# Kernel optimization log

Measured on AMD Instinct MI355X. Metric: run time of the kernel, lower is better.

## Reference

```python
import jax, jax.numpy as jnp
import numpy as np
from jax import lax

B, T, S_ENC = 64, 32, 64
E, H, V = 1024, 1024, 32000


def setup_inputs() -> dict:
    key = jax.random.key(0)
    ks = jax.random.split(key, 12)
    s = 0.02
    return {
        "inputs": jax.random.randint(ks[0], (B, T), 0, V),
        "encoder_outputs": jax.random.normal(ks[1], (B, S_ENC, 2 * H), jnp.float32),
        "h0": jax.random.normal(ks[2], (B, H), jnp.float32) * 0.1,
        "c0": jax.random.normal(ks[3], (B, H), jnp.float32) * 0.1,
        "emb": jax.random.normal(ks[4], (V, E), jnp.float32) * s,
        "W_ih": jax.random.normal(ks[5], (4 * H, E), jnp.float32) * s,
        "W_hh": jax.random.normal(ks[6], (4 * H, H), jnp.float32) * s,
        "b_ih": jnp.zeros((4 * H,), jnp.float32),
        "b_hh": jnp.zeros((4 * H,), jnp.float32),
        "attn_W": jax.random.normal(ks[7], (2 * H, H), jnp.float32) * s,  # Linear(H -> 2H, no bias)
        "comb_W": jax.random.normal(ks[8], (H, 3 * H), jnp.float32) * s,  # Linear(3H -> H)
        "comb_b": jnp.zeros((H,), jnp.float32),
        "out_W": jax.random.normal(ks[9], (V, H), jnp.float32) * s,       # Linear(H -> V)
        "out_b": jnp.zeros((V,), jnp.float32),
    }


def _decode(inputs, encoder_outputs, h0, c0, emb, W_ih, W_hh, b_ih, b_hh,
            attn_W, comb_W, comb_b, out_W, out_b):
    x = emb[inputs]                      # [B, T, E]
    bias = b_ih + b_hh

    def step(carry, x_t):
        h, c = carry                     # [B, H] each
        gates = x_t @ W_ih.T + h @ W_hh.T + bias    # [B, 4H]
        i, f, g, o = jnp.split(gates, 4, axis=-1)   # PyTorch LSTM gate order
        i, f, o = jax.nn.sigmoid(i), jax.nn.sigmoid(f), jax.nn.sigmoid(o)
        c = f * c + i * jnp.tanh(g)
        h = o * jnp.tanh(c)
        # Luong-style attention (faithful to source, incl. softmax over dim=1 of size 1)
        ah = h @ attn_W.T                                        # [B, 2H]
        scores = jnp.einsum('bd,bsd->bs', ah, encoder_outputs)[:, None, :]  # [B,1,S]
        w = jax.nn.softmax(scores, axis=1)                       # size-1 axis -> all ones
        ctx = jnp.einsum('bqs,bsd->bqd', w, encoder_outputs)[:, 0]          # [B, 2H]
        merged = jnp.concatenate([h, ctx], axis=-1)              # [B, 3H]
        out = jnp.tanh(merged @ comb_W.T + comb_b)               # [B, H]
        return (h, c), out

    (h, c), outs = lax.scan(step, (h0, c0), x.transpose(1, 0, 2))
    outputs = outs.transpose(1, 0, 2)                            # [B, T, H]
    logits = outputs @ out_W.T + out_b                           # [B, T, V]
    return logits, h, c


def reference(inputs, encoder_outputs, h0, c0, emb, W_ih, W_hh, b_ih, b_hh,
              attn_W, comb_W, comb_b, out_W, out_b):
    return _decode(inputs, encoder_outputs, h0, c0, emb, W_ih, W_hh, b_ih, b_hh,
                   attn_W, comb_W, comb_b, out_W, out_b)
```

## Files before the change

### kernel.cpp

```cpp
#include <hip/hip_runtime.h>
#include <hip/hip_bf16.h>


typedef unsigned short u16;
typedef unsigned int u32;
typedef short s8v __attribute__((ext_vector_type(8)));
typedef float f4v __attribute__((ext_vector_type(4)));

__device__ __forceinline__ u16 f2bf(float f) {
  unsigned x = __float_as_uint(f);
  return (u16)((x + 0x7fffu + ((x >> 16) & 1u)) >> 16);
}
__device__ __forceinline__ float bf2f(u16 u) {
  return __uint_as_float(((unsigned)u) << 16);
}

__device__ __forceinline__ void gl_lds16(const void* g, void* l) {
  __builtin_amdgcn_global_load_lds(
      (const __attribute__((address_space(1))) u32*)g,
      (__attribute__((address_space(3))) u32*)l, 16, 0, 0);
}

__device__ __forceinline__ int xcd_swz(int bid, int nb) {
  int q8 = nb >> 3, r8 = nb & 7;
  int xcd = bid & 7, idx = bid >> 3;
  return (xcd < r8 ? xcd * (q8 + 1) : r8 * (q8 + 1) + (xcd - r8) * q8) + idx;
}

template <int EPI>
__global__ __launch_bounds__(512, 1) void gemm_q(
    const u16* __restrict__ A, const u16* __restrict__ Bm,
    const float* __restrict__ bias, void* __restrict__ Cp,
    int K, int ldc, int gridM) {
  __shared__ __align__(16) u16 LDS[2 * 32768];

  int swz = xcd_swz((int)blockIdx.x, (int)gridDim.x);
  int mt = swz % gridM, nt = swz / gridM;
  long bm = (long)mt * 256, bn = (long)nt * 256;

  int tid = threadIdx.x;
  int w = tid >> 6, l = tid & 63;
  int wm = w & 1, wn = w >> 1;
  int lr = l & 15, lg = l >> 4;

  int nt_k = K >> 6;

  auto stage = [&](int s, int kt_idx) {
    int kt = kt_idx << 6;
    u16* sa = &LDS[s * 32768];
    u16* sb = &LDS[s * 32768 + 16384];
#pragma unroll
    for (int ch = 0; ch < 4; ++ch) {
      int cb = ch * 512 + w * 64;
      int c = cb + l;
      int row = c >> 3, sp = c & 7;
      int ko = kt + ((sp ^ (row & 7)) << 3);
      gl_lds16(A + (bm + row) * (long)K + ko, sa + cb * 8);
      gl_lds16(Bm + (bn + row) * (long)K + ko, sb + cb * 8);
    }
  };

  f4v acc[8][4];
#pragma unroll
  for (int i = 0; i < 8; ++i)
#pragma unroll
    for (int j = 0; j < 4; ++j) acc[i][j] = (f4v){0.f, 0.f, 0.f, 0.f};

  stage(0, 0);
  asm volatile("s_waitcnt vmcnt(0)" ::: "memory");
  __builtin_amdgcn_s_barrier();
  __builtin_amdgcn_sched_barrier(0);

  for (int t = 0; t < nt_k; ++t) {
    if (t + 1 < nt_k) stage((t + 1) & 1, t + 1);
    const u16* sa = &LDS[(t & 1) * 32768];
    const u16* sb = &LDS[(t & 1) * 32768 + 16384];
#pragma unroll
    for (int ks = 0; ks < 2; ++ks) {
      s8v av[8], bv[4];
#pragma unroll
      for (int i = 0; i < 8; ++i) {
        int ra = wm * 128 + i * 16 + lr;
        int pa = (ks * 4 + lg) ^ (ra & 7);
        av[i] = *(const s8v*)((const char*)sa + ra * 128 + pa * 16);
      }
#pragma unroll
      for (int i = 0; i < 4; ++i) {
        int rb = wn * 64 + i * 16 + lr;
        int pb = (ks * 4 + lg) ^ (rb & 7);
        bv[i] = *(const s8v*)((const char*)sb + rb * 128 + pb * 16);
      }
      __builtin_amdgcn_s_setprio(1);
#pragma unroll
      for (int mi = 0; mi < 8; ++mi)
#pragma unroll
        for (int ni = 0; ni < 4; ++ni)
          acc[mi][ni] = __builtin_amdgcn_mfma_f32_16x16x32_bf16(
              av[mi], bv[ni], acc[mi][ni], 0, 0, 0);
      __builtin_amdgcn_s_setprio(0);
    }
    if (t + 1 >= nt_k) break;
    asm volatile("s_waitcnt vmcnt(0)" ::: "memory");
    __builtin_amdgcn_s_barrier();
    __builtin_amdgcn_sched_barrier(0);
  }

#pragma unroll
  for (int mi = 0; mi < 8; ++mi) {
#pragma unroll
    for (int q = 0; q < 4; ++q) {
      long row = bm + wm * 128 + mi * 16 + lg * 4 + q;
#pragma unroll
      for (int ni = 0; ni < 4; ++ni) {
        long col = bn + wn * 64 + ni * 16 + lr;
        float v = acc[mi][ni][q] + bias[col];
        if (EPI == 3)
          ((float*)Cp)[row * (long)ldc + col] = v;
        else
          ((u16*)Cp)[row * (long)ldc + col] = f2bf(v);
      }
    }
  }
}

template <int EPI>
__global__ __launch_bounds__(512, 1) void gemm_p(
    const u16* __restrict__ A, const u16* __restrict__ Bm,
    const float* __restrict__ bias, void* __restrict__ Cp,
    int K, int ldc, int gridM) {
  __shared__ __align__(16) u16 LDS[3 * 24576];

  int swz = xcd_swz((int)blockIdx.x, (int)gridDim.x);
  int mt = swz % gridM, nt = swz / gridM;
  long bm = (long)mt * 128, bn = (long)nt * 256;

  int tid = threadIdx.x;
  int w = tid >> 6, l = tid & 63;
  int wm = w & 1, wn = w >> 1;
  int lr = l & 15, lg = l >> 4;

  int nt_k = K >> 6;

  auto stage = [&](int s, int kt_idx) {
    int kt = kt_idx << 6;
    u16* sa = &LDS[s * 24576];
    u16* sb = &LDS[s * 24576 + 8192];
#pragma unroll
    for (int ch = 0; ch < 2; ++ch) {
      int cb = ch * 512 + w * 64;
      int c = cb + l;
      int row = c >> 3, sp = c & 7;
      gl_lds16(A + (bm + row) * (long)K + kt + ((sp ^ (row & 7)) << 3),
               sa + cb * 8);
    }
#pragma unroll
    for (int ch = 0; ch < 4; ++ch) {
      int cb = ch * 512 + w * 64;
      int c = cb + l;
      int row = c >> 3, sp = c & 7;
      gl_lds16(Bm + (bn + row) * (long)K + kt + ((sp ^ (row & 7)) << 3),
               sb + cb * 8);
    }
  };

  f4v acc[4][4];
#pragma unroll
  for (int i = 0; i < 4; ++i)
#pragma unroll
    for (int j = 0; j < 4; ++j) acc[i][j] = (f4v){0.f, 0.f, 0.f, 0.f};

  stage(0, 0);
  stage(1, 1);
  asm volatile("s_waitcnt vmcnt(6)" ::: "memory");
  __builtin_amdgcn_s_barrier();
  __builtin_amdgcn_sched_barrier(0);

  for (int t = 0; t < nt_k; ++t) {
    if (t + 2 < nt_k) stage((t + 2) % 3, t + 2);
    const u16* sa = &LDS[(t % 3) * 24576];
    const u16* sb = &LDS[(t % 3) * 24576 + 8192];
#pragma unroll
    for (int ks = 0; ks < 2; ++ks) {
      s8v av[4], bv[4];
#pragma unroll
      for (int i = 0; i < 4; ++i) {
        int ra = wm * 64 + i * 16 + lr;
        int pa = (ks * 4 + lg) ^ (ra & 7);
        av[i] = *(const s8v*)((const char*)sa + ra * 128 + pa * 16);
        int rb = wn * 64 + i * 16 + lr;
        int pb = (ks * 4 + lg) ^ (rb & 7);
        bv[i] = *(const s8v*)((const char*)sb + rb * 128 + pb * 16);
      }
      __builtin_amdgcn_s_setprio(1);
#pragma unroll
      for (int mi = 0; mi < 4; ++mi)
#pragma unroll
        for (int ni = 0; ni < 4; ++ni)
          acc[mi][ni] = __builtin_amdgcn_mfma_f32_16x16x32_bf16(
              av[mi], bv[ni], acc[mi][ni], 0, 0, 0);
      __builtin_amdgcn_s_setprio(0);
    }
    if (t + 1 >= nt_k) break;
    if (t + 2 < nt_k) {
      asm volatile("s_waitcnt vmcnt(6)" ::: "memory");
    } else {
      asm volatile("s_waitcnt vmcnt(0)" ::: "memory");
    }
    __builtin_amdgcn_s_barrier();
    __builtin_amdgcn_sched_barrier(0);
  }

#pragma unroll
  for (int mi = 0; mi < 4; ++mi) {
#pragma unroll
    for (int q = 0; q < 4; ++q) {
      long row = bm + wm * 64 + mi * 16 + lg * 4 + q;
#pragma unroll
      for (int ni = 0; ni < 4; ++ni) {
        long col = bn + wn * 64 + ni * 16 + lr;
        float v = acc[mi][ni][q] + bias[col];
        if (EPI == 3)
          ((float*)Cp)[row * (long)ldc + col] = v;
        else
          ((u16*)Cp)[row * (long)ldc + col] = f2bf(v);
      }
    }
  }
}

template <int EPI>
__global__ __launch_bounds__(256, 2) void gemm_bt2(
    const u16* __restrict__ A, const u16* __restrict__ Bm,
    const float* __restrict__ bias, void* __restrict__ Cp,
    int K, int ldc, int gridM) {
  __shared__ __align__(16) u16 As[128 * 64];
  __shared__ __align__(16) u16 Bs[128 * 64];

  int swz = xcd_swz((int)blockIdx.x, (int)gridDim.x);
  int mt = swz % gridM, nt = swz / gridM;
  long bm = (long)mt * 128, bn = (long)nt * 128;

  int tid = threadIdx.x;
  int w = tid >> 6, l = tid & 63;
  int wm = (w & 1) * 64, wn = (w >> 1) * 64;
  int lr = l & 15, lg = l >> 4;

  f4v acc[4][4];
#pragma unroll
  for (int i = 0; i < 4; ++i)
#pragma unroll
    for (int j = 0; j < 4; ++j) acc[i][j] = (f4v){0.f, 0.f, 0.f, 0.f};

  for (int kt = 0; kt < K; kt += 64) {
#pragma unroll
    for (int p = 0; p < 4; ++p) {
      int cb = (p * 4 + w) * 64;
      int c = cb + l;
      int row = c >> 3, ce = (c & 7) * 8;
      gl_lds16(A + (bm + row) * (long)K + kt + ce, &As[cb * 8]);
      gl_lds16(Bm + (bn + row) * (long)K + kt + ce, &Bs[cb * 8]);
    }
    __syncthreads();
#pragma unroll
    for (int ks = 0; ks < 2; ++ks) {
      int kb = ks * 64 + lg * 16;
      s8v av[4], bv[4];
#pragma unroll
      for (int i = 0; i < 4; ++i) {
        av[i] = *(const s8v*)((const char*)&As[0] + (wm + i * 16 + lr) * 128 + kb);
        bv[i] = *(const s8v*)((const char*)&Bs[0] + (wn + i * 16 + lr) * 128 + kb);
      }
#pragma unroll
      for (int mi = 0; mi < 4; ++mi)
#pragma unroll
        for (int ni = 0; ni < 4; ++ni)
          acc[mi][ni] = __builtin_amdgcn_mfma_f32_16x16x32_bf16(
              av[mi], bv[ni], acc[mi][ni], 0, 0, 0);
    }
    __syncthreads();
  }
#pragma unroll
  for (int mi = 0; mi < 4; ++mi) {
#pragma unroll
    for (int q = 0; q < 4; ++q) {
      long row = bm + wm + mi * 16 + lg * 4 + q;
#pragma unroll
      for (int ni = 0; ni < 4; ++ni) {
        long col = bn + wn + ni * 16 + lr;
        float v = acc[mi][ni][q] + bias[col];
        if (EPI == 2) v = tanhf(v);
        if (EPI == 3)
          ((float*)Cp)[row * (long)ldc + col] = v;
        else
          ((u16*)Cp)[row * (long)ldc + col] = f2bf(v);
      }
    }
  }
}

template <int EPI>
__global__ __launch_bounds__(256, 2) void gemm_btf(
    const u16* __restrict__ A, const float* __restrict__ Bm,
    const float* __restrict__ bias, void* __restrict__ Cp,
    int K, int ldc, int gridM) {
  __shared__ __align__(16) u16 As[128][72];
  __shared__ __align__(16) u16 Bs[128][72];
  int swz = xcd_swz((int)blockIdx.x, (int)gridDim.x);
  int mt = swz % gridM, nt = swz / gridM;
  long bm = (long)mt * 128, bn = (long)nt * 128;
  int tid = threadIdx.x;
  int w = tid >> 6, l = tid & 63;
  int wm = (w & 1) * 64, wn = (w >> 1) * 64;
  int lr = l & 15, lg = l >> 4;
  f4v acc[4][4];
#pragma unroll
  for (int i = 0; i < 4; ++i)
#pragma unroll
    for (int j = 0; j < 4; ++j) acc[i][j] = (f4v){0.f, 0.f, 0.f, 0.f};
  for (int kt = 0; kt < K; kt += 64) {
#pragma unroll
    for (int p = 0; p < 4; ++p) {
      int ch = p * 256 + tid;
      int row = ch >> 3, cc = ch & 7;
      *(uint4*)((char*)(&As[0][0]) + row * 144 + cc * 16) =
          *(const uint4*)(A + (bm + row) * (long)K + kt + cc * 8);
      const float* bp = Bm + (bn + row) * (long)K + kt + cc * 8;
      float4 b0 = *(const float4*)bp;
      float4 b1 = *(const float4*)(bp + 4);
      union { u16 t8[8]; uint4 v; } cv;
      cv.t8[0] = f2bf(b0.x); cv.t8[1] = f2bf(b0.y);
      cv.t8[2] = f2bf(b0.z); cv.t8[3] = f2bf(b0.w);
      cv.t8[4] = f2bf(b1.x); cv.t8[5] = f2bf(b1.y);
      cv.t8[6] = f2bf(b1.z); cv.t8[7] = f2bf(b1.w);
      *(uint4*)((char*)(&Bs[0][0]) + row * 144 + cc * 16) = cv.v;
    }
    __syncthreads();
#pragma unroll
    for (int ks = 0; ks < 2; ++ks) {
      int kb = ks * 64 + lg * 16;
      s8v av[4], bv[4];
#pragma unroll
      for (int i = 0; i < 4; ++i) {
        av[i] = *(const s8v*)((const char*)(&As[0][0]) + (wm + i * 16 + lr) * 144 + kb);
        bv[i] = *(const s8v*)((const char*)(&Bs[0][0]) + (wn + i * 16 + lr) * 144 + kb);
      }
#pragma unroll
      for (int mi = 0; mi < 4; ++mi)
#pragma unroll
        for (int ni = 0; ni < 4; ++ni)
          acc[mi][ni] = __builtin_amdgcn_mfma_f32_16x16x32_bf16(
              av[mi], bv[ni], acc[mi][ni], 0, 0, 0);
    }
    __syncthreads();
  }
#pragma unroll
  for (int mi = 0; mi < 4; ++mi) {
#pragma unroll
    for (int q = 0; q < 4; ++q) {
      long row = bm + wm + mi * 16 + lg * 4 + q;
#pragma unroll
      for (int ni = 0; ni < 4; ++ni) {
        long col = bn + wn + ni * 16 + lr;
        float v = acc[mi][ni][q] + bias[col];
        if (EPI == 2) v = tanhf(v);
        if (EPI == 3)
          ((float*)Cp)[row * (long)ldc + col] = v;
        else
          ((u16*)Cp)[row * (long)ldc + col] = f2bf(v);
      }
    }
  }
}

__global__ __launch_bounds__(256, 1) void lstm_step3(
    const u16* __restrict__ Whh, const u16* __restrict__ xproj,
    const u16* __restrict__ h_in, u16* __restrict__ h_next,
    float* __restrict__ c_buf, u16* __restrict__ a2,
    float* __restrict__ hf, float* __restrict__ cf, int t) {
  __shared__ __align__(16) u16 Hs[32 * 1024];
  __shared__ __align__(16) u16 Ws[32 * 1024];
  __shared__ float Gs[32][33];

  int bid = blockIdx.x;
  int j = bid & 127, bh = bid >> 7;
  int colbase = j * 8;
  int tid = threadIdx.x, w = tid >> 6, l = tid & 63;
  int bq = w & 1, nh = w >> 1;
  int lr = l & 15, lg = l >> 4;

  int hi = tid >> 7;
  int ps = tid & 127;
#pragma unroll
  for (int p = 0; p < 16; ++p) {
    int r = 2 * p + hi;
    int sl = ps ^ (r & 7);
    gl_lds16(h_in + (bh * 32 + r) * 1024 + sl * 8, &Hs[(p * 4 + w) * 512]);
    int g = r >> 3, rr = r & 7;
    gl_lds16(Whh + (long)(g * 1024 + colbase + rr) * 1024 + sl * 8,
             &Ws[(p * 4 + w) * 512]);
  }
  __syncthreads();

  int ar = bq * 16 + lr;
  int br = nh * 16 + lr;
  int axor = (ar & 7), bxor = (br & 7);
  f4v acc0 = {0.f, 0.f, 0.f, 0.f}, acc1 = {0.f, 0.f, 0.f, 0.f};
#pragma unroll
  for (int kc = 0; kc < 32; kc += 2) {
    {
      int s = kc * 4 + lg;
      s8v av = *(const s8v*)((const char*)Hs + ar * 2048 + (s ^ axor) * 16);
      s8v bv = *(const s8v*)((const char*)Ws + br * 2048 + (s ^ bxor) * 16);
      acc0 = __builtin_amdgcn_mfma_f32_16x16x32_bf16(av, bv, acc0, 0, 0, 0);
    }
    {
      int s = (kc + 1) * 4 + lg;
      s8v av = *(const s8v*)((const char*)Hs + ar * 2048 + (s ^ axor) * 16);
      s8v bv = *(const s8v*)((const char*)Ws + br * 2048 + (s ^ bxor) * 16);
      acc1 = __builtin_amdgcn_mfma_f32_16x16x32_bf16(av, bv, acc1, 0, 0, 0);
    }
  }
#pragma unroll
  for (int q = 0; q < 4; ++q)
    Gs[bq * 16 + lg * 4 + q][nh * 16 + lr] = acc0[q] + acc1[q];
  __syncthreads();

  int b = tid >> 3, rr = tid & 7;
  int gb = bh * 32 + b;
  int col = colbase + rr;
  const u16* xp = xproj + (long)(gb * 32 + t) * 4096;
  float pi = Gs[b][rr]      + bf2f(xp[col]);
  float pf = Gs[b][8 + rr]  + bf2f(xp[1024 + col]);
  float pg = Gs[b][16 + rr] + bf2f(xp[2048 + col]);
  float po = Gs[b][24 + rr] + bf2f(xp[3072 + col]);
  float iv = 1.f / (1.f + expf(-pi));
  float fv = 1.f / (1.f + expf(-pf));
  float ov = 1.f / (1.f + expf(-po));
  float gv = tanhf(pg);
  float co = c_buf[gb * 1024 + col];
  float cn = fv * co + iv * gv;
  float hn = ov * tanhf(cn);
  c_buf[gb * 1024 + col] = cn;
  u16 hb = f2bf(hn);
  h_next[gb * 1024 + col] = hb;
  a2[(long)(gb * 32 + t) * 3072 + col] = hb;
  if (t == 31) {
    hf[gb * 1024 + col] = hn;
    cf[gb * 1024 + col] = cn;
  }
}

__global__ void k_misc(const float* __restrict__ bih, const float* __restrict__ bhh,
                       const float* __restrict__ h0, const float* __restrict__ c0,
                       float* __restrict__ bias, u16* __restrict__ hbuf0,
                       float* __restrict__ cbuf) {
  int i = blockIdx.x * 256 + threadIdx.x;
  if (i < 4096) bias[i] = bih[i] + bhh[i];
  if (i < 65536) {
    hbuf0[i] = f2bf(h0[i]);
    cbuf[i] = c0[i];
  }
}

__global__ void k_cvt8(const float* __restrict__ src, u16* __restrict__ dst, int n8) {
  int i = blockIdx.x * 256 + threadIdx.x;
  if (i >= n8) return;
  const float4* s = (const float4*)(src + (long)i * 8);
  float4 a = s[0], b = s[1];
  union { u16 t[8]; uint4 v; } cv;
  cv.t[0] = f2bf(a.x); cv.t[1] = f2bf(a.y); cv.t[2] = f2bf(a.z); cv.t[3] = f2bf(a.w);
  cv.t[4] = f2bf(b.x); cv.t[5] = f2bf(b.y); cv.t[6] = f2bf(b.z); cv.t[7] = f2bf(b.w);
  ((uint4*)dst)[i] = cv.v;
}

__global__ void k_emb8(const int* __restrict__ inp, const float* __restrict__ emb,
                       u16* __restrict__ dst) {
  int i = blockIdx.x * 256 + threadIdx.x;
  int r = i >> 7, k8 = (i & 127) * 8;
  const float* s = emb + (long)inp[r] * 1024 + k8;
  float4 a = *(const float4*)s, b = *(const float4*)(s + 4);
  union { u16 t[8]; uint4 v; } cv;
  cv.t[0] = f2bf(a.x); cv.t[1] = f2bf(a.y); cv.t[2] = f2bf(a.z); cv.t[3] = f2bf(a.w);
  cv.t[4] = f2bf(b.x); cv.t[5] = f2bf(b.y); cv.t[6] = f2bf(b.z); cv.t[7] = f2bf(b.w);
  ((uint4*)dst)[i] = cv.v;
}

__global__ void k_ctx2(const float* __restrict__ enc, u16* __restrict__ a2) {
  int b = blockIdx.x;
  int dg = threadIdx.x;
  float s[8] = {0.f, 0.f, 0.f, 0.f, 0.f, 0.f, 0.f, 0.f};
  for (int si = 0; si < 64; ++si) {
    const float* p = enc + ((long)(b * 64 + si)) * 2048 + dg * 8;
    float4 x = *(const float4*)p, y = *(const float4*)(p + 4);
    s[0] += x.x; s[1] += x.y; s[2] += x.z; s[3] += x.w;
    s[4] += y.x; s[5] += y.y; s[6] += y.z; s[7] += y.w;
  }
  union { u16 t[8]; uint4 v; } cv;
#pragma unroll
  for (int e = 0; e < 8; ++e) cv.t[e] = f2bf(s[e]);
  for (int t = 0; t < 32; ++t)
    *(uint4*)(a2 + (long)(b * 32 + t) * 3072 + 1024 + dg * 8) = cv.v;
}

extern "C" void kernel_launch(void* const* d_in, const int* in_sizes, int n_in,
                              void* d_out, int out_size, void* d_ws, size_t ws_size,
                              hipStream_t stream) {
  (void)in_sizes; (void)n_in; (void)out_size;
  const int*   inputs = (const int*)d_in[0];
  const float* enc    = (const float*)d_in[1];
  const float* h0     = (const float*)d_in[2];
  const float* c0     = (const float*)d_in[3];
  const float* emb    = (const float*)d_in[4];
  const float* Wih    = (const float*)d_in[5];
  const float* Whh    = (const float*)d_in[6];
  const float* bih    = (const float*)d_in[7];
  const float* bhh    = (const float*)d_in[8];
  const float* combW  = (const float*)d_in[10];
  const float* combb  = (const float*)d_in[11];
  const float* outW   = (const float*)d_in[12];
  const float* outb   = (const float*)d_in[13];
  float* out = (float*)d_out;

  char* ws = (char*)d_ws;
  size_t off = 0;
  auto alloc = [&](size_t bytes) {
    char* p = ws + off;
    off += (bytes + 255) & ~(size_t)255;
    return p;
  };
  u16*   WHH_BF = (u16*)  alloc(4096ull * 1024 * 2);
  u16*   XPROJ  = (u16*)  alloc(2048ull * 4096 * 2);
  u16*   EMBX   = (u16*)  alloc(2048ull * 1024 * 2);
  u16*   A2     = (u16*)  alloc(2048ull * 3072 * 2);
  u16*   OUTS   = (u16*)  alloc(2048ull * 1024 * 2);
  float* BIAS   = (float*)alloc(4096 * 4);
  u16*   HBUF   = (u16*)  alloc(2ull * 65536 * 2);
  float* CBUF   = (float*)alloc(65536 * 4);
  u16*   WIH_BF   = (u16*)alloc(4096ull * 1024 * 2);
  u16*   COMBW_BF = (u16*)alloc(1024ull * 3072 * 2);
  size_t off_w1 = off;
  u16*   OUTW_BF  = (u16*)alloc(32000ull * 1024 * 2);
  size_t off_w2 = off;
  bool haveW1 = ws_size >= off_w1;
  bool haveW2 = ws_size >= off_w2;

  k_misc<<<dim3(256), dim3(256), 0, stream>>>(bih, bhh, h0, c0, BIAS, HBUF, CBUF);
  k_cvt8<<<dim3(2048), dim3(256), 0, stream>>>(Whh, WHH_BF, 524288);
  k_emb8<<<dim3(1024), dim3(256), 0, stream>>>(inputs, emb, EMBX);
  k_ctx2<<<dim3(64), dim3(256), 0, stream>>>(enc, A2);
  if (haveW1) {
    k_cvt8<<<dim3(2048), dim3(256), 0, stream>>>(Wih, WIH_BF, 524288);
    k_cvt8<<<dim3(1536), dim3(256), 0, stream>>>(combW, COMBW_BF, 393216);
  }
  if (haveW2)
    k_cvt8<<<dim3(16000), dim3(256), 0, stream>>>(outW, OUTW_BF, 4096000);

  if (haveW1)
    gemm_p<1><<<dim3(256), dim3(512), 0, stream>>>(EMBX, WIH_BF, BIAS, XPROJ,
                                                   1024, 4096, 16);
  else
    gemm_btf<1><<<dim3(512), dim3(256), 0, stream>>>(EMBX, Wih, BIAS, XPROJ,
                                                     1024, 4096, 16);

  for (int t = 0; t < 32; ++t) {
    u16* hin  = HBUF + (t & 1) * 65536;
    u16* hout = HBUF + ((t + 1) & 1) * 65536;
    lstm_step3<<<dim3(256), dim3(256), 0, stream>>>(
        WHH_BF, XPROJ, hin, hout, CBUF, A2,
        out + 65536000, out + 65536000 + 65536, t);
  }

  if (haveW1)
    gemm_bt2<2><<<dim3(128), dim3(256), 0, stream>>>(A2, COMBW_BF, combb, OUTS,
                                                     3072, 1024, 16);
  else
    gemm_btf<2><<<dim3(128), dim3(256), 0, stream>>>(A2, combW, combb, OUTS,
                                                     3072, 1024, 16);
  if (haveW2)
    gemm_q<3><<<dim3(1000), dim3(512), 0, stream>>>(OUTS, OUTW_BF, outb, d_out,
                                                    1024, 32000, 8);
  else
    gemm_btf<3><<<dim3(4000), dim3(256), 0, stream>>>(OUTS, outW, outb, d_out,
                                                      1024, 32000, 16);
}
```

Before: 578.5 us.

## Replace per-timestep LSTM launches with a persistent kernel using grid barriers

The 32 separate lstm_step launches become one persistent kernel of 256 blocks. Each block loads its W_hh slice into LDS once, keeps the cell state in a register, and synchronises with the other blocks through per-step atomic counters in global memory. The hidden state travels through global memory using cache-bypassing loads and stores. This removes per-launch overhead and the repeated W_hh reloads, but the kernel deadlocks if all 256 blocks cannot be resident at the same time.

New measurement: 744.9 us. +28.8%, slower.

```diff
diff --git a/kernel.cpp b/kernel.cpp
--- a/kernel.cpp
+++ b/kernel.cpp
@@ -372,13 +372,13 @@
   }
 }
 
-__global__ __launch_bounds__(256, 1) void lstm_step3(
+__global__ __launch_bounds__(256, 1) void lstm_persist(
     const u16* __restrict__ Whh, const u16* __restrict__ xproj,
-    const u16* __restrict__ h_in, u16* __restrict__ h_next,
-    float* __restrict__ c_buf, u16* __restrict__ a2,
-    float* __restrict__ hf, float* __restrict__ cf, int t) {
+    u16* __restrict__ hbuf, u16* __restrict__ a2,
+    const float* __restrict__ c0, float* __restrict__ hf,
+    float* __restrict__ cf, u32* __restrict__ ctr) {
+  __shared__ __align__(16) u16 Ws[32 * 1024];
   __shared__ __align__(16) u16 Hs[32 * 1024];
-  __shared__ __align__(16) u16 Ws[32 * 1024];
   __shared__ float Gs[32][33];
 
   int bid = blockIdx.x;
@@ -387,79 +387,126 @@
   int tid = threadIdx.x, w = tid >> 6, l = tid & 63;
   int bq = w & 1, nh = w >> 1;
   int lr = l & 15, lg = l >> 4;
-
-  int hi = tid >> 7;
-  int ps = tid & 127;
+  int hi = tid >> 7, ps = tid & 127;
+
 #pragma unroll
   for (int p = 0; p < 16; ++p) {
     int r = 2 * p + hi;
     int sl = ps ^ (r & 7);
-    gl_lds16(h_in + (bh * 32 + r) * 1024 + sl * 8, &Hs[(p * 4 + w) * 512]);
     int g = r >> 3, rr = r & 7;
     gl_lds16(Whh + (long)(g * 1024 + colbase + rr) * 1024 + sl * 8,
              &Ws[(p * 4 + w) * 512]);
   }
-  __syncthreads();
+  asm volatile("s_waitcnt vmcnt(0)" ::: "memory");
+
+  int eb = tid >> 3, er = tid & 7;
+  int gb = bh * 32 + eb, ecol = colbase + er;
+  float c_reg = c0[gb * 1024 + ecol];
 
   int ar = bq * 16 + lr;
   int br = nh * 16 + lr;
-  int axor = (ar & 7), bxor = (br & 7);
-  f4v acc0 = {0.f, 0.f, 0.f, 0.f}, acc1 = {0.f, 0.f, 0.f, 0.f};
-#pragma unroll
-  for (int kc = 0; kc < 32; kc += 2) {
+  int axor = ar & 7, bxor = br & 7;
+
+#define GLD(r, p)                                              \
+  asm volatile("global_load_dwordx4 %0, %1, off sc0 sc1"       \
+               : "=v"(r) : "v"(p) : "memory")
+
+  for (int t = 0; t < 32; ++t) {
+    const u16* h_in = hbuf + (t & 1) * 65536;
+    u16* h_out = hbuf + ((t + 1) & 1) * 65536;
+
     {
-      int s = kc * 4 + lg;
-      s8v av = *(const s8v*)((const char*)Hs + ar * 2048 + (s ^ axor) * 16);
-      s8v bv = *(const s8v*)((const char*)Ws + br * 2048 + (s ^ bxor) * 16);
-      acc0 = __builtin_amdgcn_mfma_f32_16x16x32_bf16(av, bv, acc0, 0, 0, 0);
-    }
-    {
-      int s = (kc + 1) * 4 + lg;
-      s8v av = *(const s8v*)((const char*)Hs + ar * 2048 + (s ^ axor) * 16);
-      s8v bv = *(const s8v*)((const char*)Ws + br * 2048 + (s ^ bxor) * 16);
-      acc1 = __builtin_amdgcn_mfma_f32_16x16x32_bf16(av, bv, acc1, 0, 0, 0);
-    }
-  }
-#pragma unroll
-  for (int q = 0; q < 4; ++q)
-    Gs[bq * 16 + lg * 4 + q][nh * 16 + lr] = acc0[q] + acc1[q];
-  __syncthreads();
-
-  int b = tid >> 3, rr = tid & 7;
-  int gb = bh * 32 + b;
-  int col = colbase + rr;
-  const u16* xp = xproj + (long)(gb * 32 + t) * 4096;
-  float pi = Gs[b][rr]      + bf2f(xp[col]);
-  float pf = Gs[b][8 + rr]  + bf2f(xp[1024 + col]);
-  float pg = Gs[b][16 + rr] + bf2f(xp[2048 + col]);
-  float po = Gs[b][24 + rr] + bf2f(xp[3072 + col]);
-  float iv = 1.f / (1.f + expf(-pi));
-  float fv = 1.f / (1.f + expf(-pf));
-  float ov = 1.f / (1.f + expf(-po));
-  float gv = tanhf(pg);
-  float co = c_buf[gb * 1024 + col];
-  float cn = fv * co + iv * gv;
-  float hn = ov * tanhf(cn);
-  c_buf[gb * 1024 + col] = cn;
-  u16 hb = f2bf(hn);
-  h_next[gb * 1024 + col] = hb;
-  a2[(long)(gb * 32 + t) * 3072 + col] = hb;
-  if (t == 31) {
-    hf[gb * 1024 + col] = hn;
-    cf[gb * 1024 + col] = cn;
-  }
+      auto src = [&](int it) -> const u16* {
+        int row = 2 * it + hi;
+        return h_in + (bh * 32 + row) * 1024 + ((ps ^ (row & 7)) << 3);
+      };
+      auto dst = [&](int it) -> uint4* {
+        return (uint4*)&Hs[(it * 256 + tid) * 8];
+      };
+      uint4 ra0, ra1, ra2, ra3, rb0, rb1, rb2, rb3;
+      GLD(ra0, src(0)); GLD(ra1, src(1)); GLD(ra2, src(2)); GLD(ra3, src(3));
+      GLD(rb0, src(4)); GLD(rb1, src(5)); GLD(rb2, src(6)); GLD(rb3, src(7));
+      asm volatile("s_waitcnt vmcnt(4)" ::: "memory");
+      *dst(0) = ra0; *dst(1) = ra1; *dst(2) = ra2; *dst(3) = ra3;
+      GLD(ra0, src(8)); GLD(ra1, src(9)); GLD(ra2, src(10)); GLD(ra3, src(11));
+      asm volatile("s_waitcnt vmcnt(4)" ::: "memory");
+      *dst(4) = rb0; *dst(5) = rb1; *dst(6) = rb2; *dst(7) = rb3;
+      GLD(rb0, src(12)); GLD(rb1, src(13)); GLD(rb2, src(14)); GLD(rb3, src(15));
+      asm volatile("s_waitcnt vmcnt(4)" ::: "memory");
+      *dst(8) = ra0; *dst(9) = ra1; *dst(10) = ra2; *dst(11) = ra3;
+      asm volatile("s_waitcnt vmcnt(0)" ::: "memory");
+      *dst(12) = rb0; *dst(13) = rb1; *dst(14) = rb2; *dst(15) = rb3;
+    }
+    __syncthreads();
+
+    f4v acc0 = {0.f, 0.f, 0.f, 0.f}, acc1 = {0.f, 0.f, 0.f, 0.f};
+#pragma unroll
+    for (int kc = 0; kc < 32; kc += 2) {
+      {
+        int s = kc * 4 + lg;
+        s8v av = *(const s8v*)((const char*)Hs + ar * 2048 + (s ^ axor) * 16);
+        s8v bv = *(const s8v*)((const char*)Ws + br * 2048 + (s ^ bxor) * 16);
+        acc0 = __builtin_amdgcn_mfma_f32_16x16x32_bf16(av, bv, acc0, 0, 0, 0);
+      }
+      {
+        int s = (kc + 1) * 4 + lg;
+        s8v av = *(const s8v*)((const char*)Hs + ar * 2048 + (s ^ axor) * 16);
+        s8v bv = *(const s8v*)((const char*)Ws + br * 2048 + (s ^ bxor) * 16);
+        acc1 = __builtin_amdgcn_mfma_f32_16x16x32_bf16(av, bv, acc1, 0, 0, 0);
+      }
+    }
+#pragma unroll
+    for (int q = 0; q < 4; ++q)
+      Gs[bq * 16 + lg * 4 + q][nh * 16 + lr] = acc0[q] + acc1[q];
+    __syncthreads();
+
+    const u16* xp = xproj + (long)(gb * 32 + t) * 4096;
+    float pi = Gs[eb][er]      + bf2f(xp[ecol]);
+    float pf = Gs[eb][8 + er]  + bf2f(xp[1024 + ecol]);
+    float pg = Gs[eb][16 + er] + bf2f(xp[2048 + ecol]);
+    float po = Gs[eb][24 + er] + bf2f(xp[3072 + ecol]);
+    float iv = 1.f / (1.f + expf(-pi));
+    float fv = 1.f / (1.f + expf(-pf));
+    float ov = 1.f / (1.f + expf(-po));
+    float gv = tanhf(pg);
+    c_reg = fv * c_reg + iv * gv;
+    float hn = ov * tanhf(c_reg);
+    u16 hb = f2bf(hn);
+    a2[(long)(gb * 32 + t) * 3072 + ecol] = hb;
+    if (t == 31) {
+      hf[gb * 1024 + ecol] = hn;
+      cf[gb * 1024 + ecol] = c_reg;
+    }
+    unsigned hv = hb;
+    unsigned other = (unsigned)__shfl_down((int)hv, 1);
+    if ((er & 1) == 0) {
+      unsigned packed = hv | (other << 16);
+      u16* dstp = h_out + gb * 1024 + ecol;
+      asm volatile("global_store_dword %0, %1, off sc0 sc1"
+                   :: "v"(dstp), "v"(packed) : "memory");
+    }
+
+    asm volatile("s_waitcnt vmcnt(0)" ::: "memory");
+    __syncthreads();
+    if (tid == 0) {
+      __hip_atomic_fetch_add(&ctr[t], 1u, __ATOMIC_ACQ_REL,
+                             __HIP_MEMORY_SCOPE_AGENT);
+      while (__hip_atomic_load(&ctr[t], __ATOMIC_ACQUIRE,
+                               __HIP_MEMORY_SCOPE_AGENT) < 256u)
+        __builtin_amdgcn_s_sleep(2);
+    }
+    __syncthreads();
+  }
+#undef GLD
 }
 
 __global__ void k_misc(const float* __restrict__ bih, const float* __restrict__ bhh,
-                       const float* __restrict__ h0, const float* __restrict__ c0,
-                       float* __restrict__ bias, u16* __restrict__ hbuf0,
-                       float* __restrict__ cbuf) {
+                       const float* __restrict__ h0, float* __restrict__ bias,
+                       u16* __restrict__ hbuf0, u32* __restrict__ ctr) {
   int i = blockIdx.x * 256 + threadIdx.x;
   if (i < 4096) bias[i] = bih[i] + bhh[i];
-  if (i < 65536) {
-    hbuf0[i] = f2bf(h0[i]);
-    cbuf[i] = c0[i];
-  }
+  if (i < 65536) hbuf0[i] = f2bf(h0[i]);
+  if (i < 32) ctr[i] = 0;
 }
 
 __global__ void k_cvt8(const float* __restrict__ src, u16* __restrict__ dst, int n8) {
@@ -535,7 +582,7 @@
   u16*   OUTS   = (u16*)  alloc(2048ull * 1024 * 2);
   float* BIAS   = (float*)alloc(4096 * 4);
   u16*   HBUF   = (u16*)  alloc(2ull * 65536 * 2);
-  float* CBUF   = (float*)alloc(65536 * 4);
+  u32*   CTR    = (u32*)  alloc(32 * 4);
   u16*   WIH_BF   = (u16*)alloc(4096ull * 1024 * 2);
   u16*   COMBW_BF = (u16*)alloc(1024ull * 3072 * 2);
   size_t off_w1 = off;
@@ -544,7 +591,7 @@
   bool haveW1 = ws_size >= off_w1;
   bool haveW2 = ws_size >= off_w2;
 
-  k_misc<<<dim3(256), dim3(256), 0, stream>>>(bih, bhh, h0, c0, BIAS, HBUF, CBUF);
+  k_misc<<<dim3(256), dim3(256), 0, stream>>>(bih, bhh, h0, BIAS, HBUF, CTR);
   k_cvt8<<<dim3(2048), dim3(256), 0, stream>>>(Whh, WHH_BF, 524288);
   k_emb8<<<dim3(1024), dim3(256), 0, stream>>>(inputs, emb, EMBX);
   k_ctx2<<<dim3(64), dim3(256), 0, stream>>>(enc, A2);
@@ -562,13 +609,9 @@
     gemm_btf<1><<<dim3(512), dim3(256), 0, stream>>>(EMBX, Wih, BIAS, XPROJ,
                                                      1024, 4096, 16);
 
-  for (int t = 0; t < 32; ++t) {
-    u16* hin  = HBUF + (t & 1) * 65536;
-    u16* hout = HBUF + ((t + 1) & 1) * 65536;
-    lstm_step3<<<dim3(256), dim3(256), 0, stream>>>(
-        WHH_BF, XPROJ, hin, hout, CBUF, A2,
-        out + 65536000, out + 65536000 + 65536, t);
-  }
+  lstm_persist<<<dim3(256), dim3(256), 0, stream>>>(
+      WHH_BF, XPROJ, HBUF, A2, c0,
+      out + 65536000, out + 65536000 + 65536, CTR);
 
   if (haveW1)
     gemm_bt2<2><<<dim3(128), dim3(256), 0, stream>>>(A2, COMBW_BF, combb, OUTS,
```

## Deepen output GEMM pipeline and permute xproj layout for LSTM step loads

Applied to the files above, without the earlier changes.

The large output-projection GEMM now uses a 4-stage LDS ring with K-tiles of 32 instead of 2 stages of 64, keeping three tile loads in flight with partial vmcnt waits to hide global latency. The input-projection GEMM writes its result in a permuted layout (time-major, gate-interleaved) so each LSTM step thread fetches its four gate pre-activations with one 8-byte load. That load and the cell-state read are issued before the recurrent matmul, overlapping their latency with it. The trade-offs are scattered 2-byte stores in the projection epilogue and more barriers and loop iterations in the output GEMM.

Result: faster. 566.2 us (-2.1%).

```diff
diff --git a/kernel.cpp b/kernel.cpp
--- a/kernel.cpp
+++ b/kernel.cpp
@@ -28,11 +28,11 @@
 }
 
 template <int EPI>
-__global__ __launch_bounds__(512, 1) void gemm_q(
+__global__ __launch_bounds__(512, 1) void gemm_r(
     const u16* __restrict__ A, const u16* __restrict__ Bm,
     const float* __restrict__ bias, void* __restrict__ Cp,
     int K, int ldc, int gridM) {
-  __shared__ __align__(16) u16 LDS[2 * 32768];
+  __shared__ __align__(16) u16 LDS[4 * 16384];
 
   int swz = xcd_swz((int)blockIdx.x, (int)gridDim.x);
   int mt = swz % gridM, nt = swz / gridM;
@@ -43,20 +43,20 @@
   int wm = w & 1, wn = w >> 1;
   int lr = l & 15, lg = l >> 4;
 
-  int nt_k = K >> 6;
+  int nt_k = K >> 5;
 
   auto stage = [&](int s, int kt_idx) {
-    int kt = kt_idx << 6;
-    u16* sa = &LDS[s * 32768];
-    u16* sb = &LDS[s * 32768 + 16384];
-#pragma unroll
-    for (int ch = 0; ch < 4; ++ch) {
+    int kt = kt_idx << 5;
+    u16* sa = &LDS[s * 16384];
+    u16* sb = &LDS[s * 16384 + 8192];
+#pragma unroll
+    for (int ch = 0; ch < 2; ++ch) {
       int cb = ch * 512 + w * 64;
       int c = cb + l;
-      int row = c >> 3, sp = c & 7;
-      int ko = kt + ((sp ^ (row & 7)) << 3);
-      gl_lds16(A + (bm + row) * (long)K + ko, sa + cb * 8);
-      gl_lds16(Bm + (bn + row) * (long)K + ko, sb + cb * 8);
+      int row = c >> 2, sp = c & 3;
+      int sl = sp ^ ((row >> 1) & 3);
+      gl_lds16(A + (bm + row) * (long)K + kt + sl * 8, sa + cb * 8);
+      gl_lds16(Bm + (bn + row) * (long)K + kt + sl * 8, sb + cb * 8);
     }
   };
 
@@ -67,40 +67,45 @@
     for (int j = 0; j < 4; ++j) acc[i][j] = (f4v){0.f, 0.f, 0.f, 0.f};
 
   stage(0, 0);
-  asm volatile("s_waitcnt vmcnt(0)" ::: "memory");
+  if (1 < nt_k) stage(1, 1);
+  if (2 < nt_k) stage(2, 2);
+  asm volatile("s_waitcnt vmcnt(8)" ::: "memory");
   __builtin_amdgcn_s_barrier();
   __builtin_amdgcn_sched_barrier(0);
 
   for (int t = 0; t < nt_k; ++t) {
-    if (t + 1 < nt_k) stage((t + 1) & 1, t + 1);
-    const u16* sa = &LDS[(t & 1) * 32768];
-    const u16* sb = &LDS[(t & 1) * 32768 + 16384];
-#pragma unroll
-    for (int ks = 0; ks < 2; ++ks) {
-      s8v av[8], bv[4];
-#pragma unroll
-      for (int i = 0; i < 8; ++i) {
-        int ra = wm * 128 + i * 16 + lr;
-        int pa = (ks * 4 + lg) ^ (ra & 7);
-        av[i] = *(const s8v*)((const char*)sa + ra * 128 + pa * 16);
-      }
-#pragma unroll
-      for (int i = 0; i < 4; ++i) {
-        int rb = wn * 64 + i * 16 + lr;
-        int pb = (ks * 4 + lg) ^ (rb & 7);
-        bv[i] = *(const s8v*)((const char*)sb + rb * 128 + pb * 16);
-      }
-      __builtin_amdgcn_s_setprio(1);
-#pragma unroll
-      for (int mi = 0; mi < 8; ++mi)
-#pragma unroll
-        for (int ni = 0; ni < 4; ++ni)
-          acc[mi][ni] = __builtin_amdgcn_mfma_f32_16x16x32_bf16(
-              av[mi], bv[ni], acc[mi][ni], 0, 0, 0);
-      __builtin_amdgcn_s_setprio(0);
-    }
+    if (t + 3 < nt_k) stage((t + 3) & 3, t + 3);
+    const u16* sa = &LDS[(t & 3) * 16384];
+    const u16* sb = &LDS[(t & 3) * 16384 + 8192];
+    s8v av[8], bv[4];
+#pragma unroll
+    for (int i = 0; i < 8; ++i) {
+      int ra = wm * 128 + i * 16 + lr;
+      int pa = lg ^ ((ra >> 1) & 3);
+      av[i] = *(const s8v*)((const char*)sa + ra * 64 + pa * 16);
+    }
+#pragma unroll
+    for (int i = 0; i < 4; ++i) {
+      int rb = wn * 64 + i * 16 + lr;
+      int pb = lg ^ ((rb >> 1) & 3);
+      bv[i] = *(const s8v*)((const char*)sb + rb * 64 + pb * 16);
+    }
+    __builtin_amdgcn_s_setprio(1);
+#pragma unroll
+    for (int mi = 0; mi < 8; ++mi)
+#pragma unroll
+      for (int ni = 0; ni < 4; ++ni)
+        acc[mi][ni] = __builtin_amdgcn_mfma_f32_16x16x32_bf16(
+            av[mi], bv[ni], acc[mi][ni], 0, 0, 0);
+    __builtin_amdgcn_s_setprio(0);
     if (t + 1 >= nt_k) break;
-    asm volatile("s_waitcnt vmcnt(0)" ::: "memory");
+    if (t + 3 < nt_k) {
+      asm volatile("s_waitcnt vmcnt(8)" ::: "memory");
+    } else if (t + 2 < nt_k) {
+      asm volatile("s_waitcnt vmcnt(4)" ::: "memory");
+    } else {
+      asm volatile("s_waitcnt vmcnt(0)" ::: "memory");
+    }
     __builtin_amdgcn_s_barrier();
     __builtin_amdgcn_sched_barrier(0);
   }
@@ -123,7 +128,7 @@
   }
 }
 
-template <int EPI>
+template <int EPI, int PERM>
 __global__ __launch_bounds__(512, 1) void gemm_p(
     const u16* __restrict__ A, const u16* __restrict__ Bm,
     const float* __restrict__ bias, void* __restrict__ Cp,
@@ -219,10 +224,15 @@
       for (int ni = 0; ni < 4; ++ni) {
         long col = bn + wn * 64 + ni * 16 + lr;
         float v = acc[mi][ni][q] + bias[col];
-        if (EPI == 3)
+        if (PERM) {
+          long prow = (row & 31) * 64 + (row >> 5);
+          long pcol = (col & 1023) * 4 + (col >> 10);
+          ((u16*)Cp)[prow * 4096 + pcol] = f2bf(v);
+        } else if (EPI == 3) {
           ((float*)Cp)[row * (long)ldc + col] = v;
-        else
+        } else {
           ((u16*)Cp)[row * (long)ldc + col] = f2bf(v);
+        }
       }
     }
   }
@@ -298,7 +308,7 @@
   }
 }
 
-template <int EPI>
+template <int EPI, int PERM>
 __global__ __launch_bounds__(256, 2) void gemm_btf(
     const u16* __restrict__ A, const float* __restrict__ Bm,
     const float* __restrict__ bias, void* __restrict__ Cp,
@@ -363,17 +373,22 @@
         long col = bn + wn + ni * 16 + lr;
         float v = acc[mi][ni][q] + bias[col];
         if (EPI == 2) v = tanhf(v);
-        if (EPI == 3)
+        if (PERM) {
+          long prow = (row & 31) * 64 + (row >> 5);
+          long pcol = (col & 1023) * 4 + (col >> 10);
+          ((u16*)Cp)[prow * 4096 + pcol] = f2bf(v);
+        } else if (EPI == 3) {
           ((float*)Cp)[row * (long)ldc + col] = v;
-        else
+        } else {
           ((u16*)Cp)[row * (long)ldc + col] = f2bf(v);
+        }
       }
     }
   }
 }
 
 __global__ __launch_bounds__(256, 1) void lstm_step3(
-    const u16* __restrict__ Whh, const u16* __restrict__ xproj,
+    const u16* __restrict__ Whh, const u16* __restrict__ xprojT,
     const u16* __restrict__ h_in, u16* __restrict__ h_next,
     float* __restrict__ c_buf, u16* __restrict__ a2,
     float* __restrict__ hf, float* __restrict__ cf, int t) {
@@ -399,6 +414,11 @@
     gl_lds16(Whh + (long)(g * 1024 + colbase + rr) * 1024 + sl * 8,
              &Ws[(p * 4 + w) * 512]);
   }
+
+  int eb = tid >> 3, er = tid & 7;
+  int gb = bh * 32 + eb, ecol = colbase + er;
+  uint2 xv = *(const uint2*)(xprojT + ((long)t * 64 + gb) * 4096 + ecol * 4);
+  float co = c_buf[gb * 1024 + ecol];
   __syncthreads();
 
   int ar = bq * 16 + lr;
@@ -425,28 +445,23 @@
     Gs[bq * 16 + lg * 4 + q][nh * 16 + lr] = acc0[q] + acc1[q];
   __syncthreads();
 
-  int b = tid >> 3, rr = tid & 7;
-  int gb = bh * 32 + b;
-  int col = colbase + rr;
-  const u16* xp = xproj + (long)(gb * 32 + t) * 4096;
-  float pi = Gs[b][rr]      + bf2f(xp[col]);
-  float pf = Gs[b][8 + rr]  + bf2f(xp[1024 + col]);
-  float pg = Gs[b][16 + rr] + bf2f(xp[2048 + col]);
-  float po = Gs[b][24 + rr] + bf2f(xp[3072 + col]);
+  float pi = Gs[eb][er]      + bf2f((u16)(xv.x));
+  float pf = Gs[eb][8 + er]  + bf2f((u16)(xv.x >> 16));
+  float pg = Gs[eb][16 + er] + bf2f((u16)(xv.y));
+  float po = Gs[eb][24 + er] + bf2f((u16)(xv.y >> 16));
   float iv = 1.f / (1.f + expf(-pi));
   float fv = 1.f / (1.f + expf(-pf));
   float ov = 1.f / (1.f + expf(-po));
   float gv = tanhf(pg);
-  float co = c_buf[gb * 1024 + col];
   float cn = fv * co + iv * gv;
   float hn = ov * tanhf(cn);
-  c_buf[gb * 1024 + col] = cn;
+  c_buf[gb * 1024 + ecol] = cn;
   u16 hb = f2bf(hn);
-  h_next[gb * 1024 + col] = hb;
-  a2[(long)(gb * 32 + t) * 3072 + col] = hb;
+  h_next[gb * 1024 + ecol] = hb;
+  a2[(long)(gb * 32 + t) * 3072 + ecol] = hb;
   if (t == 31) {
-    hf[gb * 1024 + col] = hn;
-    cf[gb * 1024 + col] = cn;
+    hf[gb * 1024 + ecol] = hn;
+    cf[gb * 1024 + ecol] = cn;
   }
 }
 
@@ -556,11 +571,11 @@
     k_cvt8<<<dim3(16000), dim3(256), 0, stream>>>(outW, OUTW_BF, 4096000);
 
   if (haveW1)
-    gemm_p<1><<<dim3(256), dim3(512), 0, stream>>>(EMBX, WIH_BF, BIAS, XPROJ,
-                                                   1024, 4096, 16);
+    gemm_p<1, 1><<<dim3(256), dim3(512), 0, stream>>>(EMBX, WIH_BF, BIAS, XPROJ,
+                                                      1024, 4096, 16);
   else
-    gemm_btf<1><<<dim3(512), dim3(256), 0, stream>>>(EMBX, Wih, BIAS, XPROJ,
-                                                     1024, 4096, 16);
+    gemm_btf<1, 1><<<dim3(512), dim3(256), 0, stream>>>(EMBX, Wih, BIAS, XPROJ,
+                                                        1024, 4096, 16);
 
   for (int t = 0; t < 32; ++t) {
     u16* hin  = HBUF + (t & 1) * 65536;
@@ -574,12 +589,12 @@
     gemm_bt2<2><<<dim3(128), dim3(256), 0, stream>>>(A2, COMBW_BF, combb, OUTS,
                                                      3072, 1024, 16);
   else
-    gemm_btf<2><<<dim3(128), dim3(256), 0, stream>>>(A2, combW, combb, OUTS,
-                                                     3072, 1024, 16);
+    gemm_btf<2, 0><<<dim3(128), dim3(256), 0, stream>>>(A2, combW, combb, OUTS,
+                                                        3072, 1024, 16);
   if (haveW2)
-    gemm_q<3><<<dim3(1000), dim3(512), 0, stream>>>(OUTS, OUTW_BF, outb, d_out,
+    gemm_r<3><<<dim3(1000), dim3(512), 0, stream>>>(OUTS, OUTW_BF, outb, d_out,
                                                     1024, 32000, 8);
   else
-    gemm_btf<3><<<dim3(4000), dim3(256), 0, stream>>>(OUTS, outW, outb, d_out,
-                                                      1024, 32000, 16);
-}
+    gemm_btf<3, 0><<<dim3(4000), dim3(256), 0, stream>>>(OUTS, outW, outb, d_out,
+                                                         1024, 32000, 16);
+}
```
